# Performance work log

Hardware: AMD Instinct MI355X
Metric: run time of the kernel (lower is better)

Reference implementation:

```python
import jax, jax.numpy as jnp
import numpy as np


def setup_inputs() -> dict:
    key = jax.random.key(0)
    k1, k2, k3, k4, k5, k6 = jax.random.split(key, 6)
    N, M = 4096, 4096      # data matrix
    K, D = 2048, 1024      # parameter matrix K x K, similarity matrix K x D
    Npair = 128            # size of i/j index subsets
    return {
        "actual": jax.random.normal(k1, (N, M), dtype=jnp.float32),
        "prediction": jax.random.normal(k2, (N, M), dtype=jnp.float32),
        "lamb": jnp.asarray(0.1, dtype=jnp.float32),
        "P": jax.random.normal(k3, (K, K), dtype=jnp.float32),
        "S": jax.random.normal(k4, (K, D), dtype=jnp.float32),
        "i_indices": jax.random.randint(k5, (Npair,), 0, K, dtype=jnp.int64),
        "j_indices": jax.random.randint(k6, (Npair,), 0, K, dtype=jnp.int64),
    }


def _safe_norm_rows(diff):
    # L2 norm over last axis with a zero-safe sqrt (grad is 0 at exactly-0 diffs,
    # matching torch's subgradient convention for .norm()).
    d2 = jnp.sum(diff * diff, axis=-1)
    pos = d2 > 0
    return jnp.sqrt(jnp.where(pos, d2, 1.0)) * pos


def reference(actual, prediction, lamb, P, S, i_indices, j_indices):
    # (p > 0) * clamp(p, min=0) == relu(p)
    Pp = jnp.maximum(P, 0.0)
    # penalty term: ||relu(P)||_F
    penalty = jnp.linalg.norm(Pp)
    # pairwise parameter-similarity penalty:
    # sum_{i in I, j in J} relu(P)[i,j] * || S[i,:] - S[j,:] ||_2
    Si = S[i_indices]                       # [Ni, D]
    Sj = S[j_indices]                       # [Nj, D]
    diff = Si[:, None, :] - Sj[None, :, :]  # [Ni, Nj, D]
    norms = _safe_norm_rows(diff)           # [Ni, Nj]
    Pij = Pp[i_indices[:, None], j_indices[None, :]]  # [Ni, Nj]
    parameter_penalty = jnp.sum(Pij * norms)
    data_term = jnp.linalg.norm(actual - prediction)
    return data_term + lamb * (penalty + parameter_penalty)
```

## Files before the change

### kernel.cpp

```cpp
#include <hip/hip_runtime.h>
#include <math.h>

#define NB  1024
#define TPB 256

__device__ __forceinline__ float waveReduceSum(float v) {
    #pragma unroll
    for (int off = 32; off > 0; off >>= 1)
        v += __shfl_down(v, off, 64);
    return v;
}

#define CONS(AV, PV, S) { float d_;                       \
    d_ = (AV).x - (PV).x; S += d_ * d_;                   \
    d_ = (AV).y - (PV).y; S += d_ * d_;                   \
    d_ = (AV).z - (PV).z; S += d_ * d_;                   \
    d_ = (AV).w - (PV).w; S += d_ * d_; }

#define RCONS(V, S) { float r_;                           \
    r_ = fmaxf((V).x, 0.f); S += r_ * r_;                 \
    r_ = fmaxf((V).y, 0.f); S += r_ * r_;                 \
    r_ = fmaxf((V).z, 0.f); S += r_ * r_;                 \
    r_ = fmaxf((V).w, 0.f); S += r_ * r_; }

__global__ __launch_bounds__(TPB, 4)
void fused_kernel(const float* __restrict__ a,
                  const float* __restrict__ p,
                  const float* __restrict__ Pm,
                  const float* __restrict__ S,
                  const int* __restrict__ ii,
                  const int* __restrict__ jj,
                  float* __restrict__ ws,
                  long nAP, long nP, int Npair, int D, int K)
{
    __shared__ float sm0[4], sm1[4], sm2[4];
    const int wave = threadIdx.x >> 6;
    const int lane = threadIdx.x & 63;
    const int bid  = blockIdx.x;

    const long tid    = (long)bid * TPB + threadIdx.x;
    const long stride = (long)NB * TPB;

    const float4* a4 = (const float4*)a;
    const float4* p4 = (const float4*)p;
    const long n4  = nAP >> 2;
    const long nP4 = nP  >> 2;

    float s0a = 0.f, s0b = 0.f, s0c = 0.f, s0d = 0.f;

    if (n4 == 16L * stride) {
        float4 A[2][4], Pv[2][4];
        long i = tid;
        #pragma unroll
        for (int u = 0; u < 4; ++u) {
            A[0][u]  = a4[i + u * stride];
            Pv[0][u] = p4[i + u * stride];
        }
        i += 4 * stride;
        #pragma unroll
        for (int it = 1; it < 4; ++it) {
            const int nxt = it & 1;
            const int cur = nxt ^ 1;
            #pragma unroll
            for (int u = 0; u < 4; ++u) {
                A[nxt][u]  = a4[i + u * stride];
                Pv[nxt][u] = p4[i + u * stride];
            }
            i += 4 * stride;
            __builtin_amdgcn_sched_barrier(0);
            CONS(A[cur][0], Pv[cur][0], s0a);
            CONS(A[cur][1], Pv[cur][1], s0b);
            CONS(A[cur][2], Pv[cur][2], s0c);
            CONS(A[cur][3], Pv[cur][3], s0d);
        }
        CONS(A[1][0], Pv[1][0], s0a);
        CONS(A[1][1], Pv[1][1], s0b);
        CONS(A[1][2], Pv[1][2], s0c);
        CONS(A[1][3], Pv[1][3], s0d);
    } else {
        for (long i = tid; i < n4; i += stride) {
            float4 av = a4[i], pv = p4[i];
            CONS(av, pv, s0a);
        }
    }

    const float4* P4 = (const float4*)Pm;
    float s1a = 0.f, s1b = 0.f;
    if (nP4 == 4L * stride) {
        float4 B0 = P4[tid];
        float4 B1 = P4[tid + stride];
        float4 B2 = P4[tid + 2 * stride];
        float4 B3 = P4[tid + 3 * stride];
        __builtin_amdgcn_sched_barrier(0);
        RCONS(B0, s1a); RCONS(B1, s1b);
        RCONS(B2, s1a); RCONS(B3, s1b);
    } else {
        for (long q = tid; q < nP4; q += stride) {
            float4 v = P4[q];
            RCONS(v, s1a);
        }
    }

    float s0 = waveReduceSum(s0a + s0b + s0c + s0d);
    float s1 = waveReduceSum(s1a + s1b);
    if (lane == 0) { sm0[wave] = s0; sm1[wave] = s1; }

    const long totalPairs = (long)Npair * Npair;
    const long base = ((long)bid * 4 + wave) * 4;
    float local = 0.f;

    if (D == 1024 && base + 3 < totalPairs && (base % Npair) + 3 < Npair) {
        const int ig = (int)(base / Npair);
        const int j0 = (int)(base - (long)ig * Npair);
        const int ri = ii[ig];
        const float4* Si4 = (const float4*)(S + (long)ri * D);
        float4 x0 = Si4[lane];
        float4 x1 = Si4[lane + 64];
        float4 x2 = Si4[lane + 128];
        float4 x3 = Si4[lane + 192];
        const long riK = (long)ri * K;

        float d2q[4];
        int   rjq[4];
        #pragma unroll
        for (int q = 0; q < 4; ++q) {
            const int rj = jj[j0 + q];
            rjq[q] = rj;
            const float4* Sj4 = (const float4*)(S + (long)rj * D);
            float4 y0 = Sj4[lane];
            float4 y1 = Sj4[lane + 64];
            float4 y2 = Sj4[lane + 128];
            float4 y3 = Sj4[lane + 192];
            float d2 = 0.f, e;
            e = x0.x - y0.x; d2 += e * e;
            e = x0.y - y0.y; d2 += e * e;
            e = x0.z - y0.z; d2 += e * e;
            e = x0.w - y0.w; d2 += e * e;
            e = x1.x - y1.x; d2 += e * e;
            e = x1.y - y1.y; d2 += e * e;
            e = x1.z - y1.z; d2 += e * e;
            e = x1.w - y1.w; d2 += e * e;
            e = x2.x - y2.x; d2 += e * e;
            e = x2.y - y2.y; d2 += e * e;
            e = x2.z - y2.z; d2 += e * e;
            e = x2.w - y2.w; d2 += e * e;
            e = x3.x - y3.x; d2 += e * e;
            e = x3.y - y3.y; d2 += e * e;
            e = x3.z - y3.z; d2 += e * e;
            e = x3.w - y3.w; d2 += e * e;
            d2q[q] = d2;
        }
        #pragma unroll
        for (int q = 0; q < 4; ++q)
            d2q[q] = waveReduceSum(d2q[q]);
        if (lane == 0) {
            #pragma unroll
            for (int q = 0; q < 4; ++q)
                if (d2q[q] > 0.f)
                    local += fmaxf(Pm[riK + rjq[q]], 0.f) * sqrtf(d2q[q]);
        }
    } else {
        for (long pr = base; pr < base + 4 && pr < totalPairs; ++pr) {
            int ig = (int)(pr / Npair);
            int j  = (int)(pr - (long)ig * Npair);
            int ri = ii[ig];
            int rj = jj[j];
            const float* Si = S + (long)ri * D;
            const float* Sj = S + (long)rj * D;
            float d2 = 0.f;
            for (int c = lane; c < D; c += 64) {
                float e = Si[c] - Sj[c];
                d2 += e * e;
            }
            d2 = waveReduceSum(d2);
            if (lane == 0 && d2 > 0.f)
                local += fmaxf(Pm[(long)ri * K + rj], 0.f) * sqrtf(d2);
        }
    }
    if (lane == 0) sm2[wave] = local;
    __syncthreads();
    if (threadIdx.x == 0) {
        ws[bid]          = sm0[0] + sm0[1] + sm0[2] + sm0[3];
        ws[NB + bid]     = sm1[0] + sm1[1] + sm1[2] + sm1[3];
        ws[2 * NB + bid] = sm2[0] + sm2[1] + sm2[2] + sm2[3];
    }
}

__global__ void finalize_kernel(const float* __restrict__ ws,
                                const float* __restrict__ lamb,
                                float* __restrict__ out)
{
    float a0 = 0.f, a1 = 0.f, a2 = 0.f;
    const float4* w4 = (const float4*)ws;
    for (int i = threadIdx.x; i < NB / 4; i += TPB) {
        float4 v = w4[i];
        a0 += v.x + v.y + v.z + v.w;
        float4 u = w4[NB / 4 + i];
        a1 += u.x + u.y + u.z + u.w;
        float4 t = w4[2 * (NB / 4) + i];
        a2 += t.x + t.y + t.z + t.w;
    }

    a0 = waveReduceSum(a0);
    a1 = waveReduceSum(a1);
    a2 = waveReduceSum(a2);

    __shared__ float m0[4], m1[4], m2[4];
    int wave = threadIdx.x >> 6;
    int lane = threadIdx.x & 63;
    if (lane == 0) { m0[wave] = a0; m1[wave] = a1; m2[wave] = a2; }
    __syncthreads();
    if (threadIdx.x == 0) {
        float A0 = m0[0] + m0[1] + m0[2] + m0[3];
        float A1 = m1[0] + m1[1] + m1[2] + m1[3];
        float A2 = m2[0] + m2[1] + m2[2] + m2[3];
        out[0] = sqrtf(A0) + lamb[0] * (sqrtf(A1) + A2);
    }
}

extern "C" void kernel_launch(void* const* d_in, const int* in_sizes, int n_in,
                              void* d_out, int out_size, void* d_ws, size_t ws_size,
                              hipStream_t stream) {
    const float* actual = (const float*)d_in[0];
    const float* pred   = (const float*)d_in[1];
    const float* lamb   = (const float*)d_in[2];
    const float* Pm     = (const float*)d_in[3];
    const float* S      = (const float*)d_in[4];
    const int*   ii     = (const int*)d_in[5];
    const int*   jj     = (const int*)d_in[6];
    float* out = (float*)d_out;
    float* ws  = (float*)d_ws;

    long nAP   = in_sizes[0];
    long nP    = in_sizes[3];
    int  K     = (int)lround(sqrt((double)nP));
    int  Npair = in_sizes[5];
    int  D     = (int)(in_sizes[4] / K);

    fused_kernel<<<NB, TPB, 0, stream>>>(actual, pred, Pm, S, ii, jj, ws,
                                         nAP, nP, Npair, D, K);
    finalize_kernel<<<1, TPB, 0, stream>>>(ws, lamb, out);
}
```

Baseline: 37.97 us.

## Dedicate a fifth wave per block to pairwise similarity work

New measurement: 36.63 us. 3.5% less time.

```diff
diff --git a/kernel.cpp b/kernel.cpp
--- a/kernel.cpp
+++ b/kernel.cpp
@@ -2,7 +2,8 @@
 #include <math.h>
 
 #define NB  1024
-#define TPB 256
+#define TPB 320
+#define SW  4
 
 __device__ __forceinline__ float waveReduceSum(float v) {
     #pragma unroll
@@ -23,7 +24,7 @@
     r_ = fmaxf((V).z, 0.f); S += r_ * r_;                 \
     r_ = fmaxf((V).w, 0.f); S += r_ * r_; }
 
-__global__ __launch_bounds__(TPB, 4)
+__global__ __launch_bounds__(TPB, 5)
 void fused_kernel(const float* __restrict__ a,
                   const float* __restrict__ p,
                   const float* __restrict__ Pm,
@@ -33,156 +34,161 @@
                   float* __restrict__ ws,
                   long nAP, long nP, int Npair, int D, int K)
 {
-    __shared__ float sm0[4], sm1[4], sm2[4];
+    __shared__ float sm0[SW], sm1[SW];
     const int wave = threadIdx.x >> 6;
     const int lane = threadIdx.x & 63;
     const int bid  = blockIdx.x;
 
-    const long tid    = (long)bid * TPB + threadIdx.x;
-    const long stride = (long)NB * TPB;
-
-    const float4* a4 = (const float4*)a;
-    const float4* p4 = (const float4*)p;
-    const long n4  = nAP >> 2;
-    const long nP4 = nP  >> 2;
-
-    float s0a = 0.f, s0b = 0.f, s0c = 0.f, s0d = 0.f;
-
-    if (n4 == 16L * stride) {
-        float4 A[2][4], Pv[2][4];
-        long i = tid;
-        #pragma unroll
-        for (int u = 0; u < 4; ++u) {
-            A[0][u]  = a4[i + u * stride];
-            Pv[0][u] = p4[i + u * stride];
-        }
-        i += 4 * stride;
-        #pragma unroll
-        for (int it = 1; it < 4; ++it) {
-            const int nxt = it & 1;
-            const int cur = nxt ^ 1;
+    if (wave < SW) {
+        const long sid    = (long)bid * (SW * 64) + (wave * 64 + lane);
+        const long stride = (long)NB * (SW * 64);
+
+        const float4* a4 = (const float4*)a;
+        const float4* p4 = (const float4*)p;
+        const long n4  = nAP >> 2;
+        const long nP4 = nP  >> 2;
+
+        float s0a = 0.f, s0b = 0.f, s0c = 0.f, s0d = 0.f;
+
+        if (n4 == 16L * stride) {
+            float4 A[2][4], Pv[2][4];
+            long i = sid;
             #pragma unroll
             for (int u = 0; u < 4; ++u) {
-                A[nxt][u]  = a4[i + u * stride];
-                Pv[nxt][u] = p4[i + u * stride];
+                A[0][u]  = a4[i + u * stride];
+                Pv[0][u] = p4[i + u * stride];
             }
             i += 4 * stride;
+            #pragma unroll
+            for (int it = 1; it < 4; ++it) {
+                const int nxt = it & 1;
+                const int cur = nxt ^ 1;
+                #pragma unroll
+                for (int u = 0; u < 4; ++u) {
+                    A[nxt][u]  = a4[i + u * stride];
+                    Pv[nxt][u] = p4[i + u * stride];
+                }
+                i += 4 * stride;
+                __builtin_amdgcn_sched_barrier(0);
+                CONS(A[cur][0], Pv[cur][0], s0a);
+                CONS(A[cur][1], Pv[cur][1], s0b);
+                CONS(A[cur][2], Pv[cur][2], s0c);
+                CONS(A[cur][3], Pv[cur][3], s0d);
+            }
+            CONS(A[1][0], Pv[1][0], s0a);
+            CONS(A[1][1], Pv[1][1], s0b);
+            CONS(A[1][2], Pv[1][2], s0c);
+            CONS(A[1][3], Pv[1][3], s0d);
+        } else {
+            for (long i = sid; i < n4; i += stride) {
+                float4 av = a4[i], pv = p4[i];
+                CONS(av, pv, s0a);
+            }
+        }
+
+        const float4* P4 = (const float4*)Pm;
+        float s1a = 0.f, s1b = 0.f;
+        if (nP4 == 4L * stride) {
+            float4 B0 = P4[sid];
+            float4 B1 = P4[sid + stride];
+            float4 B2 = P4[sid + 2 * stride];
+            float4 B3 = P4[sid + 3 * stride];
             __builtin_amdgcn_sched_barrier(0);
-            CONS(A[cur][0], Pv[cur][0], s0a);
-            CONS(A[cur][1], Pv[cur][1], s0b);
-            CONS(A[cur][2], Pv[cur][2], s0c);
-            CONS(A[cur][3], Pv[cur][3], s0d);
+            RCONS(B0, s1a); RCONS(B1, s1b);
+            RCONS(B2, s1a); RCONS(B3, s1b);
+        } else {
+            for (long q = sid; q < nP4; q += stride) {
+                float4 v = P4[q];
+                RCONS(v, s1a);
+            }
         }
-        CONS(A[1][0], Pv[1][0], s0a);
-        CONS(A[1][1], Pv[1][1], s0b);
-        CONS(A[1][2], Pv[1][2], s0c);
-        CONS(A[1][3], Pv[1][3], s0d);
+
+        float s0 = waveReduceSum(s0a + s0b + s0c + s0d);
+        float s1 = waveReduceSum(s1a + s1b);
+        if (lane == 0) { sm0[wave] = s0; sm1[wave] = s1; }
     } else {
-        for (long i = tid; i < n4; i += stride) {
-            float4 av = a4[i], pv = p4[i];
-            CONS(av, pv, s0a);
+        const long totalPairs = (long)Npair * Npair;
+        const long base = (long)bid * 16;
+        float local = 0.f;
+
+        if (D == 1024 && base + 15 < totalPairs && (base % Npair) + 15 < Npair) {
+            const int ig = (int)(base / Npair);
+            const int j0 = (int)(base - (long)ig * Npair);
+            const int ri = ii[ig];
+            const float4* Si4 = (const float4*)(S + (long)ri * D);
+            float4 x0 = Si4[lane];
+            float4 x1 = Si4[lane + 64];
+            float4 x2 = Si4[lane + 128];
+            float4 x3 = Si4[lane + 192];
+            const long riK = (long)ri * K;
+
+            #pragma unroll
+            for (int g = 0; g < 4; ++g) {
+                float d2q[4];
+                int   rjq[4];
+                #pragma unroll
+                for (int q = 0; q < 4; ++q) {
+                    const int rj = jj[j0 + g * 4 + q];
+                    rjq[q] = rj;
+                    const float4* Sj4 = (const float4*)(S + (long)rj * D);
+                    float4 y0 = Sj4[lane];
+                    float4 y1 = Sj4[lane + 64];
+                    float4 y2 = Sj4[lane + 128];
+                    float4 y3 = Sj4[lane + 192];
+                    float d2 = 0.f, e;
+                    e = x0.x - y0.x; d2 += e * e;
+                    e = x0.y - y0.y; d2 += e * e;
+                    e = x0.z - y0.z; d2 += e * e;
+                    e = x0.w - y0.w; d2 += e * e;
+                    e = x1.x - y1.x; d2 += e * e;
+                    e = x1.y - y1.y; d2 += e * e;
+                    e = x1.z - y1.z; d2 += e * e;
+                    e = x1.w - y1.w; d2 += e * e;
+                    e = x2.x - y2.x; d2 += e * e;
+                    e = x2.y - y2.y; d2 += e * e;
+                    e = x2.z - y2.z; d2 += e * e;
+                    e = x2.w - y2.w; d2 += e * e;
+                    e = x3.x - y3.x; d2 += e * e;
+                    e = x3.y - y3.y; d2 += e * e;
+                    e = x3.z - y3.z; d2 += e * e;
+                    e = x3.w - y3.w; d2 += e * e;
+                    d2q[q] = d2;
+                }
+                #pragma unroll
+                for (int q = 0; q < 4; ++q)
+                    d2q[q] = waveReduceSum(d2q[q]);
+                if (lane == 0) {
+                    #pragma unroll
+                    for (int q = 0; q < 4; ++q)
+                        if (d2q[q] > 0.f)
+                            local += fmaxf(Pm[riK + rjq[q]], 0.f) * sqrtf(d2q[q]);
+                }
+            }
+        } else {
+            for (long pr = base; pr < base + 16 && pr < totalPairs; ++pr) {
+                int ig = (int)(pr / Npair);
+                int j  = (int)(pr - (long)ig * Npair);
+                int ri = ii[ig];
+                int rj = jj[j];
+                const float* Si = S + (long)ri * D;
+                const float* Sj = S + (long)rj * D;
+                float d2 = 0.f;
+                for (int c = lane; c < D; c += 64) {
+                    float e = Si[c] - Sj[c];
+                    d2 += e * e;
+                }
+                d2 = waveReduceSum(d2);
+                if (lane == 0 && d2 > 0.f)
+                    local += fmaxf(Pm[(long)ri * K + rj], 0.f) * sqrtf(d2);
+            }
         }
-    }
-
-    const float4* P4 = (const float4*)Pm;
-    float s1a = 0.f, s1b = 0.f;
-    if (nP4 == 4L * stride) {
-        float4 B0 = P4[tid];
-        float4 B1 = P4[tid + stride];
-        float4 B2 = P4[tid + 2 * stride];
-        float4 B3 = P4[tid + 3 * stride];
-        __builtin_amdgcn_sched_barrier(0);
-        RCONS(B0, s1a); RCONS(B1, s1b);
-        RCONS(B2, s1a); RCONS(B3, s1b);
-    } else {
-        for (long q = tid; q < nP4; q += stride) {
-            float4 v = P4[q];
-            RCONS(v, s1a);
-        }
-    }
-
-    float s0 = waveReduceSum(s0a + s0b + s0c + s0d);
-    float s1 = waveReduceSum(s1a + s1b);
-    if (lane == 0) { sm0[wave] = s0; sm1[wave] = s1; }
-
-    const long totalPairs = (long)Npair * Npair;
-    const long base = ((long)bid * 4 + wave) * 4;
-    float local = 0.f;
-
-    if (D == 1024 && base + 3 < totalPairs && (base % Npair) + 3 < Npair) {
-        const int ig = (int)(base / Npair);
-        const int j0 = (int)(base - (long)ig * Npair);
-        const int ri = ii[ig];
-        const float4* Si4 = (const float4*)(S + (long)ri * D);
-        float4 x0 = Si4[lane];
-        float4 x1 = Si4[lane + 64];
-        float4 x2 = Si4[lane + 128];
-        float4 x3 = Si4[lane + 192];
-        const long riK = (long)ri * K;
-
-        float d2q[4];
-        int   rjq[4];
-        #pragma unroll
-        for (int q = 0; q < 4; ++q) {
-            const int rj = jj[j0 + q];
-            rjq[q] = rj;
-            const float4* Sj4 = (const float4*)(S + (long)rj * D);
-            float4 y0 = Sj4[lane];
-            float4 y1 = Sj4[lane + 64];
-            float4 y2 = Sj4[lane + 128];
-            float4 y3 = Sj4[lane + 192];
-            float d2 = 0.f, e;
-            e = x0.x - y0.x; d2 += e * e;
-            e = x0.y - y0.y; d2 += e * e;
-            e = x0.z - y0.z; d2 += e * e;
-            e = x0.w - y0.w; d2 += e * e;
-            e = x1.x - y1.x; d2 += e * e;
-            e = x1.y - y1.y; d2 += e * e;
-            e = x1.z - y1.z; d2 += e * e;
-            e = x1.w - y1.w; d2 += e * e;
-            e = x2.x - y2.x; d2 += e * e;
-            e = x2.y - y2.y; d2 += e * e;
-            e = x2.z - y2.z; d2 += e * e;
-            e = x2.w - y2.w; d2 += e * e;
-            e = x3.x - y3.x; d2 += e * e;
-            e = x3.y - y3.y; d2 += e * e;
-            e = x3.z - y3.z; d2 += e * e;
-            e = x3.w - y3.w; d2 += e * e;
-            d2q[q] = d2;
-        }
-        #pragma unroll
-        for (int q = 0; q < 4; ++q)
-            d2q[q] = waveReduceSum(d2q[q]);
-        if (lane == 0) {
-            #pragma unroll
-            for (int q = 0; q < 4; ++q)
-                if (d2q[q] > 0.f)
-                    local += fmaxf(Pm[riK + rjq[q]], 0.f) * sqrtf(d2q[q]);
-        }
-    } else {
-        for (long pr = base; pr < base + 4 && pr < totalPairs; ++pr) {
-            int ig = (int)(pr / Npair);
-            int j  = (int)(pr - (long)ig * Npair);
-            int ri = ii[ig];
-            int rj = jj[j];
-            const float* Si = S + (long)ri * D;
-            const float* Sj = S + (long)rj * D;
-            float d2 = 0.f;
-            for (int c = lane; c < D; c += 64) {
-                float e = Si[c] - Sj[c];
-                d2 += e * e;
-            }
-            d2 = waveReduceSum(d2);
-            if (lane == 0 && d2 > 0.f)
-                local += fmaxf(Pm[(long)ri * K + rj], 0.f) * sqrtf(d2);
-        }
-    }
-    if (lane == 0) sm2[wave] = local;
+        if (lane == 0) ws[2 * NB + bid] = local;
+    }
+
     __syncthreads();
     if (threadIdx.x == 0) {
-        ws[bid]          = sm0[0] + sm0[1] + sm0[2] + sm0[3];
-        ws[NB + bid]     = sm1[0] + sm1[1] + sm1[2] + sm1[3];
-        ws[2 * NB + bid] = sm2[0] + sm2[1] + sm2[2] + sm2[3];
+        ws[bid]      = sm0[0] + sm0[1] + sm0[2] + sm0[3];
+        ws[NB + bid] = sm1[0] + sm1[1] + sm1[2] + sm1[3];
     }
 }
 
@@ -192,7 +198,7 @@
 {
     float a0 = 0.f, a1 = 0.f, a2 = 0.f;
     const float4* w4 = (const float4*)ws;
-    for (int i = threadIdx.x; i < NB / 4; i += TPB) {
+    for (int i = threadIdx.x; i < NB / 4; i += 256) {
         float4 v = w4[i];
         a0 += v.x + v.y + v.z + v.w;
         float4 u = w4[NB / 4 + i];
@@ -239,5 +245,5 @@
 
     fused_kernel<<<NB, TPB, 0, stream>>>(actual, pred, Pm, S, ii, jj, ws,
                                          nAP, nP, Npair, D, K);
-    finalize_kernel<<<1, TPB, 0, stream>>>(ws, lamb, out);
-}
+    finalize_kernel<<<1, 256, 0, stream>>>(ws, lamb, out);
+}
```
